# Kernel tuning notes

Hardware: AMD Instinct MI355X
Metric: run time of the kernel (lower is better)

## Reference

```python
import jax, jax.numpy as jnp
import numpy as np

NUM_CLASSES = 80
STRIDES = (8, 16, 32)
FEATS = ((80, 80), (40, 40), (20, 20))
RADIUS = 2.5
CAND_K = 10


def make_grids():
    grids, strides = [], []
    for (h, w), s in zip(FEATS, STRIDES):
        gx, gy = jnp.meshgrid(jnp.arange(w), jnp.arange(h))  # xy indexing: gx=col, gy=row
        g = jnp.stack([gx, gy], -1).reshape(-1, 2).astype(jnp.float32)
        grids.append(g)
        strides.append(jnp.full((h * w, 1), float(s), jnp.float32))
    return jnp.concatenate(grids, 0), jnp.concatenate(strides, 0)  # [A,2], [A,1]


def decode_level(p, s):
    # p: [B, 85, h, w] -> decoded [B, h*w, 85]; xy/wh decoded, conf/cls stay logits
    b, c, h, w = p.shape
    out = p.reshape(b, c, h * w).transpose(0, 2, 1)
    gx, gy = jnp.meshgrid(jnp.arange(w), jnp.arange(h))
    g = jnp.stack([gx, gy], -1).reshape(1, -1, 2).astype(p.dtype)
    xy = (out[..., :2] + g) * s
    wh = jnp.exp(out[..., 2:4]) * s
    return jnp.concatenate([xy, wh, out[..., 4:]], -1)


def pairwise_iou_cxcywh(a, b):
    # a: [G,4], b: [A,4] -> [G,A]
    tl = jnp.maximum(a[:, None, :2] - a[:, None, 2:] * 0.5, b[None, :, :2] - b[None, :, 2:] * 0.5)
    br = jnp.minimum(a[:, None, :2] + a[:, None, 2:] * 0.5, b[None, :, :2] + b[None, :, 2:] * 0.5)
    wh = jnp.clip(br - tl, 0.0)
    inter = wh[..., 0] * wh[..., 1]
    area_a = (a[:, 2] * a[:, 3])[:, None]
    area_b = (b[:, 2] * b[:, 3])[None, :]
    return inter / (area_a + area_b - inter + 1e-16)


def elem_iou_cxcywh(a, b):
    # a, b: [...,4] aligned -> [...]
    tl = jnp.maximum(a[..., :2] - a[..., 2:] * 0.5, b[..., :2] - b[..., 2:] * 0.5)
    br = jnp.minimum(a[..., :2] + a[..., 2:] * 0.5, b[..., :2] + b[..., 2:] * 0.5)
    wh = jnp.clip(br - tl, 0.0)
    inter = wh[..., 0] * wh[..., 1]
    area = a[..., 2] * a[..., 3] + b[..., 2] * b[..., 3]
    return inter / (area - inter + 1e-16)


def bce_logits(x, t):
    return jnp.maximum(x, 0.0) - x * t + jnp.log1p(jnp.exp(-jnp.abs(x)))


def assign_one(gt_b, gt_c, pbox, pconf, pcls, xy_center, stride_v):
    # SimOTA dynamic matching for one image. gt_b:[G,4], gt_c:[G], pbox:[A,4], pconf:[A,1], pcls:[A,C]
    G = gt_b.shape[0]
    # center-in-box / center-in-mirror(radius) masks
    bmin = gt_b[:, :2] - gt_b[:, 2:] * 0.5
    bmax = gt_b[:, :2] + gt_b[:, 2:] * 0.5
    d = jnp.concatenate([xy_center[None] - bmin[:, None], bmax[:, None] - xy_center[None]], -1)  # [G,A,4]
    in_box = jnp.min(d, -1) > 0.0
    mmin = gt_b[:, None, :2] - RADIUS * stride_v[None]
    mmax = gt_b[:, None, :2] + RADIUS * stride_v[None]
    d2 = jnp.concatenate([xy_center[None] - mmin, mmax - xy_center[None]], -1)
    in_mir = jnp.min(d2, -1) > 0.0
    union = jnp.any(in_box, 0) | jnp.any(in_mir, 0)  # [A]
    inter = in_box & in_mir  # [G,A]

    iou = pairwise_iou_cxcywh(gt_b, pbox)  # [G,A]
    iou_cost = -jnp.log(iou + 1e-8)
    # cls cost: BCE(sqrt(sigmoid(cls)*sigmoid(conf)), one_hot).sum(C), computed without [G,A,C]
    p = jnp.sqrt(jax.nn.sigmoid(pcls) * jax.nn.sigmoid(pconf))  # [A,C]
    logp = jnp.clip(jnp.log(jnp.clip(p, 1e-12)), -100.0)
    log1mp = jnp.clip(jnp.log(jnp.clip(1.0 - p, 1e-12)), -100.0)
    cls_cost = -(logp[:, gt_c].T - log1mp[:, gt_c].T + log1mp.sum(-1)[None, :])  # [G,A]

    cost = cls_cost + 3.0 * iou_cost + 1e5 * (~inter).astype(cost_dtype(pcls))
    cost = jnp.where(union[None, :], cost, 1e15)  # exclude anchors outside union (bool-index in torch)
    iou_m = jnp.where(union[None, :], iou, 0.0)

    # dynamic k per gt = clamp(int(sum top10 iou), 1)
    topk_iou, _ = jax.lax.top_k(iou_m, CAND_K)
    dyn_k = jnp.maximum(topk_iou.sum(1).astype(jnp.int32), 1)  # [G]
    _, idx = jax.lax.top_k(-cost, CAND_K)  # smallest-cost anchors per gt [G,10]
    valid = (jnp.arange(CAND_K)[None, :] < dyn_k[:, None]).astype(cost.dtype)
    mm = jnp.zeros_like(cost).at[jnp.arange(G)[:, None], idx].set(valid)  # [G,A]

    # resolve anchors matched to >1 gt by argmin cost
    multi = mm.sum(0) > 1.0
    best = jnp.argmin(cost, 0)  # [A]
    mm = jnp.where(multi[None, :], jax.nn.one_hot(best, G, dtype=mm.dtype).T, mm)

    fg = mm.sum(0) > 0.0  # [A]
    gt_idx = jnp.argmax(mm, 0)  # [A]
    match_iou = (mm * iou).sum(0)  # [A]
    return fg, gt_idx, match_iou


def cost_dtype(x):
    return x.dtype


def setup_inputs() -> dict:
    key = jax.random.key(0)
    ks = jax.random.split(key, 5)
    B, G = 32, 16
    p8 = jax.random.normal(ks[0], (B, 85, 80, 80), jnp.float32)
    p16 = jax.random.normal(ks[1], (B, 85, 40, 40), jnp.float32)
    p32 = jax.random.normal(ks[2], (B, 85, 20, 20), jnp.float32)
    u = jax.random.uniform(ks[3], (B, G, 4), jnp.float32)
    gt_boxes = jnp.concatenate([32.0 + u[..., :2] * 576.0, 16.0 + u[..., 2:] * 112.0], -1)
    gt_cls = jax.random.randint(ks[4], (B, G), 0, 80, dtype=jnp.int32)
    return {"p8": p8, "p16": p16, "p32": p32, "gt_boxes": gt_boxes, "gt_cls": gt_cls}


def reference(p8, p16, p32, gt_boxes, gt_cls):
    outs = [decode_level(p, s) for p, s in zip((p8, p16, p32), STRIDES)]
    outputs = jnp.concatenate(outs, 1)  # [B, 8400, 85]
    grids, stride_v = make_grids()
    xy_center = (grids + 0.5) * stride_v  # [A,2]
    pbox, pconf, pcls = outputs[..., :4], outputs[..., 4:5], outputs[..., 5:]

    sg = jax.lax.stop_gradient  # assignment is under torch.no_grad
    fg, gt_idx, match_iou = jax.vmap(assign_one, in_axes=(0, 0, 0, 0, 0, None, None))(
        gt_boxes, gt_cls, sg(pbox), sg(pconf), sg(pcls), xy_center, stride_v)
    match_iou = sg(match_iou)

    tgt_box = jnp.take_along_axis(gt_boxes, gt_idx[..., None], axis=1)  # [B,A,4]
    tgt_cls_id = jnp.take_along_axis(gt_cls, gt_idx, axis=1)  # [B,A]
    tgt_cls = jax.nn.one_hot(tgt_cls_id, NUM_CLASSES, dtype=outputs.dtype) * match_iou[..., None]
    fgf = fg.astype(outputs.dtype)

    iou_e = elem_iou_cxcywh(pbox, tgt_box)  # [B,A]
    loss_box = jnp.sum(fgf * (1.0 - iou_e ** 2))            # IOUloss, fg only
    loss_conf = jnp.sum(bce_logits(pconf[..., 0], fgf))     # all anchors
    loss_cls = jnp.sum(fgf[..., None] * bce_logits(pcls, tgt_cls))  # fg only
    n_fg = jnp.maximum(jnp.sum(fgf), 1.0)
    return (5.0 * loss_box + loss_conf + loss_cls) / n_fg
```

## Files before the change

kernel.cpp:

```cpp
#include <hip/hip_runtime.h>
#include <hip/hip_bf16.h>

#define A_TOT 8400
#define NB 32
#define NG 16
#define NC 80

#define K1_GX 33
#define NWAVE (K1_GX * NB * 4)
#define K3_CH 8
#define K3_W  1050
#define K3_BLOCKS (K3_CH * NB)

#define L2E 1.44269504088896340736f
#define LN2 0.69314718055994530942f

__device__ inline float fexp2(float x) { return __builtin_amdgcn_exp2f(x); }
__device__ inline float flog2(float x) { return __builtin_amdgcn_logf(x); }
__device__ inline float frcp(float x)  { return __builtin_amdgcn_rcpf(x); }
__device__ inline float fsqrtf_(float x) { return __builtin_amdgcn_sqrtf(x); }

__device__ inline float iou_cxcywh(float acx, float acy, float aw, float ah,
                                   float bcx, float bcy, float bw, float bh) {
    float tlx = fmaxf(acx - aw * 0.5f, bcx - bw * 0.5f);
    float tly = fmaxf(acy - ah * 0.5f, bcy - bh * 0.5f);
    float brx = fminf(acx + aw * 0.5f, bcx + bw * 0.5f);
    float bry = fminf(acy + ah * 0.5f, bcy + bh * 0.5f);
    float w = fmaxf(brx - tlx, 0.0f);
    float h = fmaxf(bry - tly, 0.0f);
    float inter = w * h;
    return inter / (aw * ah + bw * bh - inter + 1e-16f);
}

__device__ inline float dval_of(float x, float sc) {
    float u = fexp2(-x * L2E);
    float sx = frcp(1.0f + u);
    float pr = fsqrtf_(sx * sc);
    float lp  = fmaxf(LN2 * flog2(fmaxf(pr, 1e-12f)), -100.0f);
    float l1p = fmaxf(LN2 * flog2(fmaxf(1.0f - pr, 1e-12f)), -100.0f);
    return lp - l1p;
}

__device__ inline float cost_fast(float iou, float d, float sp, unsigned m, int g) {
    if (!((m >> 16) & 1u)) return 1e15f;
    float c = -(d + sp) - 3.0f * LN2 * flog2(iou + 1e-8f);
    if (!((m >> g) & 1u)) c += 100000.0f;
    return c;
}

__device__ inline unsigned long long umax64(unsigned long long a, unsigned long long b) {
    return a > b ? a : b;
}
__device__ inline unsigned long long umin64(unsigned long long a, unsigned long long b) {
    return a < b ? a : b;
}

__device__ inline const float* lvl_base(int a, int b, const float* p8, const float* p16,
                                        const float* p32, int& hw, int& HW, int& W, float& s) {
    if (a < 6400) { hw = a;        HW = 6400; W = 80; s = 8.0f;  return p8  + (size_t)b * 85 * 6400; }
    if (a < 8000) { hw = a - 6400; HW = 1600; W = 40; s = 16.0f; return p16 + (size_t)b * 85 * 1600; }
    { hw = a - 8000; HW = 400; W = 20; s = 32.0f; return p32 + (size_t)b * 85 * 400; }
}

__global__ __launch_bounds__(256) void k1_decode(
    const float* __restrict__ p8, const float* __restrict__ p16, const float* __restrict__ p32,
    const float* __restrict__ gtb,
    float4* __restrict__ pbox, float4* __restrict__ rec,
    int* __restrict__ cmp, int* __restrict__ cnt, float* __restrict__ part) {
    __shared__ int lcnt, base_s;
    int b = blockIdx.y;
    int tid = threadIdx.x;
    int a = blockIdx.x * 256 + tid;
    if (tid == 0) lcnt = 0;
    __syncthreads();

    float bce0_conf = 0.0f;
    int myslot = -1;
    if (a < A_TOT) {
        int hw, HW, W;
        float s;
        const float* base = lvl_base(a, b, p8, p16, p32, hw, HW, W, s);

        float tx = base[hw], ty = base[HW + hw];
        float tw = base[2 * HW + hw], th = base[3 * HW + hw];
        float cf = base[4 * HW + hw];
        int gx = hw % W, gy = hw / W;
        float pcx = (tx + (float)gx) * s;
        float pcy = (ty + (float)gy) * s;
        float pw = fexp2(tw * L2E) * s;
        float ph = fexp2(th * L2E) * s;

        float uc = fexp2(-cf * L2E);
        float suc = 1.0f + uc;
        float sc = frcp(suc);
        bce0_conf = cf + LN2 * flog2(suc);

        float xc = ((float)gx + 0.5f) * s;
        float yc = ((float)gy + 0.5f) * s;
        unsigned m = 0;
        bool uni = false;
        float r = 2.5f * s;
#pragma unroll 4
        for (int g = 0; g < NG; g++) {
            float gcx = gtb[(b * NG + g) * 4 + 0];
            float gcy = gtb[(b * NG + g) * 4 + 1];
            float gw  = gtb[(b * NG + g) * 4 + 2];
            float gh  = gtb[(b * NG + g) * 4 + 3];
            bool ib = (xc > gcx - gw * 0.5f) && (gcx + gw * 0.5f > xc) &&
                      (yc > gcy - gh * 0.5f) && (gcy + gh * 0.5f > yc);
            bool im = (xc > gcx - r) && (gcx + r > xc) &&
                      (yc > gcy - r) && (gcy + r > yc);
            uni |= (ib || im);
            if (ib && im) m |= (1u << g);
        }
        if (uni) m |= (1u << 16);

        float suml1p = 0.0f;
        if (uni) {
            myslot = atomicAdd(&lcnt, 1);
            const float* cbase = base + 5 * HW + hw;
#pragma unroll
            for (int cc = 0; cc < NC; cc += 20) {
                float x[20];
#pragma unroll
                for (int j = 0; j < 20; j++) x[j] = cbase[(cc + j) * HW];
#pragma unroll
                for (int j = 0; j < 20; j++) {
                    float u = fexp2(-x[j] * L2E);
                    float pr = fsqrtf_(frcp(1.0f + u) * sc);
                    suml1p += fmaxf(LN2 * flog2(fmaxf(1.0f - pr, 1e-12f)), -100.0f);
                }
            }
        }

        size_t i = (size_t)b * A_TOT + a;
        pbox[i] = make_float4(pcx, pcy, pw, ph);
        rec[i] = make_float4(__uint_as_float(m), sc, suml1p, cf);
    }
    __syncthreads();
    if (tid == 0) base_s = atomicAdd(&cnt[b], lcnt);
    __syncthreads();
    if (myslot >= 0) cmp[(size_t)b * A_TOT + base_s + myslot] = a;

    float v = bce0_conf;
    for (int off = 32; off; off >>= 1) v += __shfl_down(v, off, 64);
    if ((tid & 63) == 0) {
        int wave = (blockIdx.y * gridDim.x + blockIdx.x) * 4 + (tid >> 6);
        part[wave] = v;
    }
}

__global__ __launch_bounds__(256, 4) void k2_assign(
    const float* __restrict__ gtb, const int* __restrict__ gtc,
    const float4* __restrict__ pbox, const float4* __restrict__ rec,
    const int* __restrict__ cmp, const int* __restrict__ cnt,
    const float* __restrict__ p8, const float* __restrict__ p16, const float* __restrict__ p32,
    int* __restrict__ sel, int* __restrict__ nsel) {
    __shared__ unsigned long long wred[4];
    int blk = blockIdx.x;
    int b = blk >> 4, g = blk & 15;
    int tid = threadIdx.x;

    float gcx = gtb[blk * 4 + 0], gcy = gtb[blk * 4 + 1];
    float gw = gtb[blk * 4 + 2],  gh = gtb[blk * 4 + 3];
    int cg = gtc[blk];
    int n = cnt[b];

    unsigned long long topI[10];
    unsigned long long topC[10];
#pragma unroll
    for (int i = 0; i < 10; i++) { topI[i] = 0ull; topC[i] = 0xFFFFFFFFFFFFFFFFull; }

    for (int j = tid; j < n; j += 256) {
        int a = cmp[(size_t)b * A_TOT + j];
        size_t i = (size_t)b * A_TOT + a;
        float4 pb = pbox[i];
        float4 rc = rec[i];
        unsigned m = __float_as_uint(rc.x);
        float iou = iou_cxcywh(gcx, gcy, gw, gh, pb.x, pb.y, pb.z, pb.w);

        int hw, HW, W;
        float s;
        const float* base = lvl_base(a, b, p8, p16, p32, hw, HW, W, s);
        float x = base[(5 + cg) * HW + hw];
        float d = dval_of(x, rc.y);
        float cost = -(d + rc.z) - 3.0f * LN2 * flog2(iou + 1e-8f);
        if (!((m >> g) & 1u)) cost += 100000.0f;

        if (iou > 0.0f) {
            unsigned long long kI = ((unsigned long long)__float_as_uint(iou) << 32) | (unsigned)a;
            if (kI > topI[9]) {
                unsigned long long v = kI;
#pragma unroll
                for (int i2 = 0; i2 < 10; i2++) {
                    unsigned long long big = umax64(topI[i2], v);
                    v = umin64(topI[i2], v);
                    topI[i2] = big;
                }
            }
        }
        unsigned long long kC = ((unsigned long long)__float_as_uint(cost) << 32) | (unsigned)a;
        if (kC < topC[9]) {
            unsigned long long v = kC;
#pragma unroll
            for (int i2 = 0; i2 < 10; i2++) {
                unsigned long long sml = umin64(topC[i2], v);
                v = umax64(topC[i2], v);
                topC[i2] = sml;
            }
        }
    }

    float ksum = 0.0f;
    for (int rr = 0; rr < 10; rr++) {
        unsigned long long h = topI[0];
        for (int off = 32; off; off >>= 1) h = umax64(h, __shfl_xor(h, off, 64));
        if ((tid & 63) == 0) wred[tid >> 6] = h;
        __syncthreads();
        unsigned long long w = umax64(umax64(wred[0], wred[1]), umax64(wred[2], wred[3]));
        ksum += __uint_as_float((unsigned)(w >> 32));
        if (topI[0] == w) {
#pragma unroll
            for (int i = 0; i < 9; i++) topI[i] = topI[i + 1];
            topI[9] = 0ull;
        }
        __syncthreads();
    }
    int dynk = (int)ksum;
    if (dynk < 1) dynk = 1;
    if (dynk > 10) dynk = 10;

    for (int rr = 0; rr < 10; rr++) {
        unsigned long long h = topC[0];
        for (int off = 32; off; off >>= 1) h = umin64(h, __shfl_xor(h, off, 64));
        if ((tid & 63) == 0) wred[tid >> 6] = h;
        __syncthreads();
        unsigned long long w = umin64(umin64(wred[0], wred[1]), umin64(wred[2], wred[3]));
        if (tid == 0) sel[blk * 10 + rr] = (int)(w & 0xffffffffu);
        if (topC[0] == w) {
#pragma unroll
            for (int i = 0; i < 9; i++) topC[i] = topC[i + 1];
            topC[9] = 0xFFFFFFFFFFFFFFFFull;
        }
        __syncthreads();
    }
    if (tid == 0) nsel[blk] = dynk;
}

__global__ __launch_bounds__(256) void k3_resolve(
    const float* __restrict__ gtb, const int* __restrict__ gtc,
    const float4* __restrict__ pbox, const float4* __restrict__ rec,
    const int* __restrict__ sel, const int* __restrict__ nsel,
    const float* __restrict__ p8, const float* __restrict__ p16, const float* __restrict__ p32,
    float4* __restrict__ part3) {
    __shared__ unsigned tag[K3_W];
    __shared__ float gb[NG * 4];
    __shared__ int gc[NG];
    __shared__ float red[256];
    int b = blockIdx.y, chunk = blockIdx.x, tid = threadIdx.x;
    int a0 = chunk * K3_W;

    for (int j = tid; j < K3_W; j += 256) tag[j] = 0;
    if (tid < NG * 4) gb[tid] = gtb[b * NG * 4 + tid];
    if (tid < NG) gc[tid] = gtc[b * NG + tid];
    __syncthreads();

    if (tid < NG * 10) {
        int g = tid / 10, k = tid % 10;
        if (k < nsel[b * NG + g]) {
            int a = sel[(b * NG + g) * 10 + k];
            if (a >= a0 && a < a0 + K3_W)
                atomicAdd(&tag[a - a0], 0x10000u + (unsigned)(g + 1));
        }
    }
    __syncthreads();

    float lbox = 0.0f, lconfc = 0.0f, lcls = 0.0f, nfg = 0.0f;
    for (int j = tid; j < K3_W; j += 256) {
        unsigned t = tag[j];
        unsigned cnt2 = t >> 16;
        if (!cnt2) continue;
        int a = a0 + j;
        size_t i = (size_t)b * A_TOT + a;
        float4 pb = pbox[i];
        float4 rc = rec[i];
        int hw, HW, W;
        float s;
        const float* base = lvl_base(a, b, p8, p16, p32, hw, HW, W, s);
        int gs;
        if (cnt2 == 1) {
            gs = (int)(t & 0xffffu) - 1;
        } else {
            unsigned m = __float_as_uint(rc.x);
            float bc = 3.402823466e38f;
            gs = 0;
            for (int g = 0; g < NG; g++) {
                float iou = iou_cxcywh(gb[g * 4], gb[g * 4 + 1], gb[g * 4 + 2], gb[g * 4 + 3],
                                       pb.x, pb.y, pb.z, pb.w);
                float x = base[(5 + gc[g]) * HW + hw];
                float d = dval_of(x, rc.y);
                float c = cost_fast(iou, d, rc.z, m, g);
                if (c < bc) { bc = c; gs = g; }
            }
        }
        float miou = iou_cxcywh(gb[gs * 4], gb[gs * 4 + 1], gb[gs * 4 + 2], gb[gs * 4 + 3],
                                pb.x, pb.y, pb.z, pb.w);
        int cid = gc[gs];
        float xcid = base[(5 + cid) * HW + hw];

        float s0 = 0.0f;
        const float* cbase = base + 5 * HW + hw;
#pragma unroll
        for (int cc = 0; cc < NC; cc += 20) {
            float x[20];
#pragma unroll
            for (int jj = 0; jj < 20; jj++) x[jj] = cbase[(cc + jj) * HW];
#pragma unroll
            for (int jj = 0; jj < 20; jj++) {
                float u = fexp2(-x[jj] * L2E);
                s0 += x[jj] + LN2 * flog2(1.0f + u);
            }
        }

        lbox += 1.0f - miou * miou;
        lconfc -= rc.w;
        lcls += s0 - xcid * miou;
        nfg += 1.0f;
    }

    float vals[4] = {lbox, lconfc, lcls, nfg};
    float outv[4];
    for (int i = 0; i < 4; i++) {
        red[tid] = vals[i];
        __syncthreads();
        for (int s2 = 128; s2 > 0; s2 >>= 1) {
            if (tid < s2) red[tid] += red[tid + s2];
            __syncthreads();
        }
        outv[i] = red[0];
        __syncthreads();
    }
    if (tid == 0)
        part3[b * K3_CH + chunk] = make_float4(outv[0], outv[1], outv[2], outv[3]);
}

__global__ __launch_bounds__(256) void k4_final(
    const float* __restrict__ part, const float4* __restrict__ part3, float* __restrict__ out) {
    __shared__ float red[256];
    int tid = threadIdx.x;
    float v = 0.0f;
    for (int i = tid; i < NWAVE; i += 256) v += part[i];
    float4 p = part3[tid];
    float vals[5] = {v, p.x, p.y, p.z, p.w};
    float tot[5];
    for (int i = 0; i < 5; i++) {
        red[tid] = vals[i];
        __syncthreads();
        for (int s2 = 128; s2 > 0; s2 >>= 1) {
            if (tid < s2) red[tid] += red[tid + s2];
            __syncthreads();
        }
        tot[i] = red[0];
        __syncthreads();
    }
    if (tid == 0) {
        float nfg = tot[4];
        if (nfg < 1.0f) nfg = 1.0f;
        out[0] = (5.0f * tot[1] + (tot[0] + tot[2]) + tot[3]) / nfg;
    }
}

extern "C" void kernel_launch(void* const* d_in, const int* in_sizes, int n_in,
                              void* d_out, int out_size, void* d_ws, size_t ws_size,
                              hipStream_t stream) {
    const float* p8  = (const float*)d_in[0];
    const float* p16 = (const float*)d_in[1];
    const float* p32 = (const float*)d_in[2];
    const float* gtb = (const float*)d_in[3];
    const int*   gtc = (const int*)d_in[4];

    char* w = (char*)d_ws;
    float4* pbox = (float4*)w;                 w += (size_t)NB * A_TOT * sizeof(float4);
    float4* rec  = (float4*)w;                 w += (size_t)NB * A_TOT * sizeof(float4);
    int* cmp     = (int*)w;                    w += (size_t)NB * A_TOT * sizeof(int);
    int* sel     = (int*)w;                    w += (size_t)NB * NG * 10 * sizeof(int);
    int* nsel    = (int*)w;                    w += (size_t)NB * NG * sizeof(int);
    float* part  = (float*)w;                  w += (size_t)NWAVE * sizeof(float);
    float4* part3 = (float4*)w;                w += (size_t)K3_BLOCKS * sizeof(float4);
    int* cnt     = (int*)w;                    w += (size_t)NB * sizeof(int);

    hipMemsetAsync(cnt, 0, NB * sizeof(int), stream);
    k1_decode<<<dim3(K1_GX, NB), 256, 0, stream>>>(
        p8, p16, p32, gtb, pbox, rec, cmp, cnt, part);
    k2_assign<<<NB * NG, 256, 0, stream>>>(gtb, gtc, pbox, rec, cmp, cnt,
                                           p8, p16, p32, sel, nsel);
    k3_resolve<<<dim3(K3_CH, NB), 256, 0, stream>>>(gtb, gtc, pbox, rec,
                                                    sel, nsel, p8, p16, p32, part3);
    k4_final<<<1, 256, 0, stream>>>(part, part3, (float*)d_out);
}
```

Before: 174.7 us.

## Fuse assign and resolve kernels into per-image block with segmented compaction

Merges the per-GT top-k assignment kernel and the conflict-resolution kernel into one 1024-thread block per image. Each GT is handled by one wavefront, so block-level syncs in the top-k reductions become pure wave shuffles, and the selections stay in shared memory. The first kernel now writes compacted candidate records per block segment and no longer needs the global counter atomic or the memset. Only candidates get box decode and global writes, and the resolve stage recomputes boxes from the raw inputs. The cost is that only 32 blocks are launched for the heavy phase, which sharply reduces parallelism on a large GPU, and the segmented scan loops over padded slots.

```diff
diff --git a/kernel.cpp b/kernel.cpp
--- a/kernel.cpp
+++ b/kernel.cpp
@@ -7,10 +7,8 @@
 #define NC 80
 
 #define K1_GX 33
+#define SEG   (K1_GX * 256)
 #define NWAVE (K1_GX * NB * 4)
-#define K3_CH 8
-#define K3_W  1050
-#define K3_BLOCKS (K3_CH * NB)
 
 #define L2E 1.44269504088896340736f
 #define LN2 0.69314718055994530942f
@@ -41,13 +39,6 @@
     return lp - l1p;
 }
 
-__device__ inline float cost_fast(float iou, float d, float sp, unsigned m, int g) {
-    if (!((m >> 16) & 1u)) return 1e15f;
-    float c = -(d + sp) - 3.0f * LN2 * flog2(iou + 1e-8f);
-    if (!((m >> g) & 1u)) c += 100000.0f;
-    return c;
-}
-
 __device__ inline unsigned long long umax64(unsigned long long a, unsigned long long b) {
     return a > b ? a : b;
 }
@@ -65,9 +56,9 @@
 __global__ __launch_bounds__(256) void k1_decode(
     const float* __restrict__ p8, const float* __restrict__ p16, const float* __restrict__ p32,
     const float* __restrict__ gtb,
-    float4* __restrict__ pbox, float4* __restrict__ rec,
+    float4* __restrict__ pbox_c, float4* __restrict__ rec_c,
     int* __restrict__ cmp, int* __restrict__ cnt, float* __restrict__ part) {
-    __shared__ int lcnt, base_s;
+    __shared__ int lcnt;
     int b = blockIdx.y;
     int tid = threadIdx.x;
     int a = blockIdx.x * 256 + tid;
@@ -75,26 +66,18 @@
     __syncthreads();
 
     float bce0_conf = 0.0f;
-    int myslot = -1;
     if (a < A_TOT) {
         int hw, HW, W;
         float s;
         const float* base = lvl_base(a, b, p8, p16, p32, hw, HW, W, s);
 
-        float tx = base[hw], ty = base[HW + hw];
-        float tw = base[2 * HW + hw], th = base[3 * HW + hw];
         float cf = base[4 * HW + hw];
-        int gx = hw % W, gy = hw / W;
-        float pcx = (tx + (float)gx) * s;
-        float pcy = (ty + (float)gy) * s;
-        float pw = fexp2(tw * L2E) * s;
-        float ph = fexp2(th * L2E) * s;
-
         float uc = fexp2(-cf * L2E);
         float suc = 1.0f + uc;
         float sc = frcp(suc);
         bce0_conf = cf + LN2 * flog2(suc);
 
+        int gx = hw % W, gy = hw / W;
         float xc = ((float)gx + 0.5f) * s;
         float yc = ((float)gy + 0.5f) * s;
         unsigned m = 0;
@@ -113,11 +96,16 @@
             uni |= (ib || im);
             if (ib && im) m |= (1u << g);
         }
-        if (uni) m |= (1u << 16);
-
-        float suml1p = 0.0f;
         if (uni) {
-            myslot = atomicAdd(&lcnt, 1);
+            m |= (1u << 16);
+            int myslot = atomicAdd(&lcnt, 1);
+            float tx = base[hw], ty = base[HW + hw];
+            float tw = base[2 * HW + hw], th = base[3 * HW + hw];
+            float pcx = (tx + (float)gx) * s;
+            float pcy = (ty + (float)gy) * s;
+            float pw = fexp2(tw * L2E) * s;
+            float ph = fexp2(th * L2E) * s;
+            float suml1p = 0.0f;
             const float* cbase = base + 5 * HW + hw;
 #pragma unroll
             for (int cc = 0; cc < NC; cc += 20) {
@@ -131,16 +119,14 @@
                     suml1p += fmaxf(LN2 * flog2(fmaxf(1.0f - pr, 1e-12f)), -100.0f);
                 }
             }
-        }
-
-        size_t i = (size_t)b * A_TOT + a;
-        pbox[i] = make_float4(pcx, pcy, pw, ph);
-        rec[i] = make_float4(__uint_as_float(m), sc, suml1p, cf);
-    }
-    __syncthreads();
-    if (tid == 0) base_s = atomicAdd(&cnt[b], lcnt);
-    __syncthreads();
-    if (myslot >= 0) cmp[(size_t)b * A_TOT + base_s + myslot] = a;
+            int slot = b * SEG + blockIdx.x * 256 + myslot;
+            pbox_c[slot] = make_float4(pcx, pcy, pw, ph);
+            rec_c[slot] = make_float4(__uint_as_float(m), sc, suml1p, cf);
+            cmp[slot] = a;
+        }
+    }
+    __syncthreads();
+    if (tid == 0) cnt[b * K1_GX + blockIdx.x] = lcnt;
 
     float v = bce0_conf;
     for (int off = 32; off; off >>= 1) v += __shfl_down(v, off, 64);
@@ -150,32 +136,45 @@
     }
 }
 
-__global__ __launch_bounds__(256, 4) void k2_assign(
+__global__ __launch_bounds__(1024, 4) void k23_assign_resolve(
     const float* __restrict__ gtb, const int* __restrict__ gtc,
-    const float4* __restrict__ pbox, const float4* __restrict__ rec,
+    const float4* __restrict__ pbox_c, const float4* __restrict__ rec_c,
     const int* __restrict__ cmp, const int* __restrict__ cnt,
     const float* __restrict__ p8, const float* __restrict__ p16, const float* __restrict__ p32,
-    int* __restrict__ sel, int* __restrict__ nsel) {
-    __shared__ unsigned long long wred[4];
-    int blk = blockIdx.x;
-    int b = blk >> 4, g = blk & 15;
+    float4* __restrict__ part3) {
+    __shared__ unsigned tag[A_TOT];
+    __shared__ int cnt_s[K1_GX];
+    __shared__ int sel_s[NG * 10];
+    __shared__ int nsel_s[NG];
+    __shared__ float gb[NG * 4];
+    __shared__ int gc[NG];
+    __shared__ float red[1024];
+    int b = blockIdx.x;
     int tid = threadIdx.x;
-
-    float gcx = gtb[blk * 4 + 0], gcy = gtb[blk * 4 + 1];
-    float gw = gtb[blk * 4 + 2],  gh = gtb[blk * 4 + 3];
-    int cg = gtc[blk];
-    int n = cnt[b];
+    int g = tid >> 6;
+    int lane = tid & 63;
+
+    if (tid < K1_GX) cnt_s[tid] = cnt[b * K1_GX + tid];
+    if (tid < NG * 4) gb[tid] = gtb[b * NG * 4 + tid];
+    if (tid < NG) gc[tid] = gtc[b * NG + tid];
+    for (int j = tid; j < A_TOT; j += 1024) tag[j] = 0;
+    __syncthreads();
+
+    float gcx = gb[g * 4], gcy = gb[g * 4 + 1];
+    float gw = gb[g * 4 + 2], gh = gb[g * 4 + 3];
+    int cg = gc[g];
 
     unsigned long long topI[10];
     unsigned long long topC[10];
 #pragma unroll
     for (int i = 0; i < 10; i++) { topI[i] = 0ull; topC[i] = 0xFFFFFFFFFFFFFFFFull; }
 
-    for (int j = tid; j < n; j += 256) {
-        int a = cmp[(size_t)b * A_TOT + j];
-        size_t i = (size_t)b * A_TOT + a;
-        float4 pb = pbox[i];
-        float4 rc = rec[i];
+    for (int j = lane; j < SEG; j += 64) {
+        if ((j & 255) >= cnt_s[j >> 8]) continue;
+        int slot = b * SEG + j;
+        float4 pb = pbox_c[slot];
+        float4 rc = rec_c[slot];
+        int a = cmp[slot];
         unsigned m = __float_as_uint(rc.x);
         float iou = iou_cxcywh(gcx, gcy, gw, gh, pb.x, pb.y, pb.z, pb.w);
 
@@ -212,99 +211,86 @@
     }
 
     float ksum = 0.0f;
+#pragma unroll
     for (int rr = 0; rr < 10; rr++) {
-        unsigned long long h = topI[0];
-        for (int off = 32; off; off >>= 1) h = umax64(h, __shfl_xor(h, off, 64));
-        if ((tid & 63) == 0) wred[tid >> 6] = h;
-        __syncthreads();
-        unsigned long long w = umax64(umax64(wred[0], wred[1]), umax64(wred[2], wred[3]));
+        unsigned long long w = topI[0];
+        for (int off = 32; off; off >>= 1) w = umax64(w, __shfl_xor(w, off, 64));
         ksum += __uint_as_float((unsigned)(w >> 32));
         if (topI[0] == w) {
 #pragma unroll
             for (int i = 0; i < 9; i++) topI[i] = topI[i + 1];
             topI[9] = 0ull;
         }
-        __syncthreads();
     }
     int dynk = (int)ksum;
     if (dynk < 1) dynk = 1;
     if (dynk > 10) dynk = 10;
 
+#pragma unroll
     for (int rr = 0; rr < 10; rr++) {
-        unsigned long long h = topC[0];
-        for (int off = 32; off; off >>= 1) h = umin64(h, __shfl_xor(h, off, 64));
-        if ((tid & 63) == 0) wred[tid >> 6] = h;
-        __syncthreads();
-        unsigned long long w = umin64(umin64(wred[0], wred[1]), umin64(wred[2], wred[3]));
-        if (tid == 0) sel[blk * 10 + rr] = (int)(w & 0xffffffffu);
+        unsigned long long w = topC[0];
+        for (int off = 32; off; off >>= 1) w = umin64(w, __shfl_xor(w, off, 64));
+        if (lane == 0) sel_s[g * 10 + rr] = (int)(w & 0xffffffffu);
         if (topC[0] == w) {
 #pragma unroll
             for (int i = 0; i < 9; i++) topC[i] = topC[i + 1];
             topC[9] = 0xFFFFFFFFFFFFFFFFull;
         }
-        __syncthreads();
-    }
-    if (tid == 0) nsel[blk] = dynk;
-}
-
-__global__ __launch_bounds__(256) void k3_resolve(
-    const float* __restrict__ gtb, const int* __restrict__ gtc,
-    const float4* __restrict__ pbox, const float4* __restrict__ rec,
-    const int* __restrict__ sel, const int* __restrict__ nsel,
-    const float* __restrict__ p8, const float* __restrict__ p16, const float* __restrict__ p32,
-    float4* __restrict__ part3) {
-    __shared__ unsigned tag[K3_W];
-    __shared__ float gb[NG * 4];
-    __shared__ int gc[NG];
-    __shared__ float red[256];
-    int b = blockIdx.y, chunk = blockIdx.x, tid = threadIdx.x;
-    int a0 = chunk * K3_W;
-
-    for (int j = tid; j < K3_W; j += 256) tag[j] = 0;
-    if (tid < NG * 4) gb[tid] = gtb[b * NG * 4 + tid];
-    if (tid < NG) gc[tid] = gtc[b * NG + tid];
+    }
+    if (lane == 0) nsel_s[g] = dynk;
     __syncthreads();
 
     if (tid < NG * 10) {
-        int g = tid / 10, k = tid % 10;
-        if (k < nsel[b * NG + g]) {
-            int a = sel[(b * NG + g) * 10 + k];
-            if (a >= a0 && a < a0 + K3_W)
-                atomicAdd(&tag[a - a0], 0x10000u + (unsigned)(g + 1));
-        }
+        int g2 = tid / 10, k = tid % 10;
+        if (k < nsel_s[g2])
+            atomicAdd(&tag[sel_s[g2 * 10 + k]], 0x10000u + (unsigned)(g2 + 1));
     }
     __syncthreads();
 
     float lbox = 0.0f, lconfc = 0.0f, lcls = 0.0f, nfg = 0.0f;
-    for (int j = tid; j < K3_W; j += 256) {
-        unsigned t = tag[j];
+    for (int a = tid; a < A_TOT; a += 1024) {
+        unsigned t = tag[a];
         unsigned cnt2 = t >> 16;
         if (!cnt2) continue;
-        int a = a0 + j;
-        size_t i = (size_t)b * A_TOT + a;
-        float4 pb = pbox[i];
-        float4 rc = rec[i];
         int hw, HW, W;
         float s;
         const float* base = lvl_base(a, b, p8, p16, p32, hw, HW, W, s);
+        float tx = base[hw], ty = base[HW + hw];
+        float tw = base[2 * HW + hw], th = base[3 * HW + hw];
+        float cf = base[4 * HW + hw];
+        int gx = hw % W, gy = hw / W;
+        float pcx = (tx + (float)gx) * s;
+        float pcy = (ty + (float)gy) * s;
+        float pw = fexp2(tw * L2E) * s;
+        float ph = fexp2(th * L2E) * s;
+
         int gs;
         if (cnt2 == 1) {
             gs = (int)(t & 0xffffu) - 1;
         } else {
-            unsigned m = __float_as_uint(rc.x);
+            float sc = frcp(1.0f + fexp2(-cf * L2E));
+            float xc = ((float)gx + 0.5f) * s;
+            float yc = ((float)gy + 0.5f) * s;
+            float r = 2.5f * s;
             float bc = 3.402823466e38f;
             gs = 0;
-            for (int g = 0; g < NG; g++) {
-                float iou = iou_cxcywh(gb[g * 4], gb[g * 4 + 1], gb[g * 4 + 2], gb[g * 4 + 3],
-                                       pb.x, pb.y, pb.z, pb.w);
-                float x = base[(5 + gc[g]) * HW + hw];
-                float d = dval_of(x, rc.y);
-                float c = cost_fast(iou, d, rc.z, m, g);
-                if (c < bc) { bc = c; gs = g; }
+            for (int g2 = 0; g2 < NG; g2++) {
+                float bx = gb[g2 * 4], by = gb[g2 * 4 + 1];
+                float bw = gb[g2 * 4 + 2], bh = gb[g2 * 4 + 3];
+                float iou = iou_cxcywh(bx, by, bw, bh, pcx, pcy, pw, ph);
+                float x = base[(5 + gc[g2]) * HW + hw];
+                float d = dval_of(x, sc);
+                float c = -d - 3.0f * LN2 * flog2(iou + 1e-8f);
+                bool ib = (xc > bx - bw * 0.5f) && (bx + bw * 0.5f > xc) &&
+                          (yc > by - bh * 0.5f) && (by + bh * 0.5f > yc);
+                bool im = (xc > bx - r) && (bx + r > xc) &&
+                          (yc > by - r) && (by + r > yc);
+                if (!(ib && im)) c += 100000.0f;
+                if (c < bc) { bc = c; gs = g2; }
             }
         }
         float miou = iou_cxcywh(gb[gs * 4], gb[gs * 4 + 1], gb[gs * 4 + 2], gb[gs * 4 + 3],
-                                pb.x, pb.y, pb.z, pb.w);
+                                pcx, pcy, pw, ph);
         int cid = gc[gs];
         float xcid = base[(5 + cid) * HW + hw];
 
@@ -323,7 +309,7 @@
         }
 
         lbox += 1.0f - miou * miou;
-        lconfc -= rc.w;
+        lconfc -= cf;
         lcls += s0 - xcid * miou;
         nfg += 1.0f;
     }
@@ -333,15 +319,14 @@
     for (int i = 0; i < 4; i++) {
         red[tid] = vals[i];
         __syncthreads();
-        for (int s2 = 128; s2 > 0; s2 >>= 1) {
+        for (int s2 = 512; s2 > 0; s2 >>= 1) {
             if (tid < s2) red[tid] += red[tid + s2];
             __syncthreads();
         }
         outv[i] = red[0];
         __syncthreads();
     }
-    if (tid == 0)
-        part3[b * K3_CH + chunk] = make_float4(outv[0], outv[1], outv[2], outv[3]);
+    if (tid == 0) part3[b] = make_float4(outv[0], outv[1], outv[2], outv[3]);
 }
 
 __global__ __launch_bounds__(256) void k4_final(
@@ -350,7 +335,7 @@
     int tid = threadIdx.x;
     float v = 0.0f;
     for (int i = tid; i < NWAVE; i += 256) v += part[i];
-    float4 p = part3[tid];
+    float4 p = (tid < NB) ? part3[tid] : make_float4(0.f, 0.f, 0.f, 0.f);
     float vals[5] = {v, p.x, p.y, p.z, p.w};
     float tot[5];
     for (int i = 0; i < 5; i++) {
@@ -380,21 +365,16 @@
     const int*   gtc = (const int*)d_in[4];
 
     char* w = (char*)d_ws;
-    float4* pbox = (float4*)w;                 w += (size_t)NB * A_TOT * sizeof(float4);
-    float4* rec  = (float4*)w;                 w += (size_t)NB * A_TOT * sizeof(float4);
-    int* cmp     = (int*)w;                    w += (size_t)NB * A_TOT * sizeof(int);
-    int* sel     = (int*)w;                    w += (size_t)NB * NG * 10 * sizeof(int);
-    int* nsel    = (int*)w;                    w += (size_t)NB * NG * sizeof(int);
-    float* part  = (float*)w;                  w += (size_t)NWAVE * sizeof(float);
-    float4* part3 = (float4*)w;                w += (size_t)K3_BLOCKS * sizeof(float4);
-    int* cnt     = (int*)w;                    w += (size_t)NB * sizeof(int);
-
-    hipMemsetAsync(cnt, 0, NB * sizeof(int), stream);
+    float4* pbox_c = (float4*)w;               w += (size_t)NB * SEG * sizeof(float4);
+    float4* rec_c  = (float4*)w;               w += (size_t)NB * SEG * sizeof(float4);
+    int* cmp       = (int*)w;                  w += (size_t)NB * SEG * sizeof(int);
+    int* cnt       = (int*)w;                  w += (size_t)NB * K1_GX * sizeof(int);
+    float* part    = (float*)w;                w += (size_t)NWAVE * sizeof(float);
+    float4* part3  = (float4*)w;               w += (size_t)NB * sizeof(float4);
+
     k1_decode<<<dim3(K1_GX, NB), 256, 0, stream>>>(
-        p8, p16, p32, gtb, pbox, rec, cmp, cnt, part);
-    k2_assign<<<NB * NG, 256, 0, stream>>>(gtb, gtc, pbox, rec, cmp, cnt,
-                                           p8, p16, p32, sel, nsel);
-    k3_resolve<<<dim3(K3_CH, NB), 256, 0, stream>>>(gtb, gtc, pbox, rec,
-                                                    sel, nsel, p8, p16, p32, part3);
+        p8, p16, p32, gtb, pbox_c, rec_c, cmp, cnt, part);
+    k23_assign_resolve<<<NB, 1024, 0, stream>>>(gtb, gtc, pbox_c, rec_c, cmp, cnt,
+                                                p8, p16, p32, part3);
     k4_final<<<1, 256, 0, stream>>>(part, part3, (float*)d_out);
 }
```

Measured after the change: 235.8 us. 34.9% more time.
